# Optimization experiments

Hardware: AMD Instinct MI355X
Metric: run time of the kernel (lower is better)

## Reference

```python
import jax, jax.numpy as jnp
import numpy as np

B, S, D = 4, 2048, 1024
H = 16
DH = D // H


def setup_inputs() -> dict:
    key = jax.random.key(0)
    ks = jax.random.split(key, 9)
    s = 0.02
    return {
        "x": jax.random.normal(ks[0], (B, S, D), dtype=jnp.float32),
        "Wq": jax.random.normal(ks[1], (D, D), dtype=jnp.float32) * s,
        "bq": jax.random.normal(ks[2], (D,), dtype=jnp.float32) * s,
        "Wk": jax.random.normal(ks[3], (D, D), dtype=jnp.float32) * s,
        "bk": jax.random.normal(ks[4], (D,), dtype=jnp.float32) * s,
        "Wv": jax.random.normal(ks[5], (D, D), dtype=jnp.float32) * s,
        "bv": jax.random.normal(ks[6], (D,), dtype=jnp.float32) * s,
        "Wo": jax.random.normal(ks[7], (D, D), dtype=jnp.float32) * s,
        "bo": jax.random.normal(ks[8], (D,), dtype=jnp.float32) * s,
    }


def _split_heads(t):
    # [B,S,D] -> [B,H,S,DH]
    b, s, d = t.shape
    return t.reshape(b, s, H, DH).transpose(0, 2, 1, 3)


def reference(x, Wq, bq, Wk, bk, Wv, bv, Wo, bo):
    q = _split_heads(x @ Wq.T + bq)
    k = _split_heads(x @ Wk.T + bk)
    v = _split_heads(x @ Wv.T + bv)
    scale = 1.0 / np.sqrt(DH).astype(np.float32)
    scores = jnp.einsum("bhqd,bhkd->bhqk", q, k) * scale  # [B,H,S,S]
    s = scores.shape[-2]
    causal = jnp.tril(jnp.ones((s, s), dtype=bool))
    scores = jnp.where(causal[None, None], scores, -jnp.inf)
    probs = jax.nn.softmax(scores, axis=-1)
    out = jnp.einsum("bhqk,bhkd->bhqd", probs, v)  # [B,H,S,DH]
    out = out.transpose(0, 2, 1, 3).reshape(x.shape[0], s, D)
    return out @ Wo.T + bo
```

## Files before the change

kernel.cpp:

```cpp
#include <hip/hip_runtime.h>
#include <hip/hip_bf16.h>
#include <cstdint>
#include <cstddef>


typedef unsigned short u16;
typedef __bf16 bf16x8 __attribute__((ext_vector_type(8)));
typedef float  f32x4  __attribute__((ext_vector_type(4)));

__device__ __forceinline__ u16 f2bf(float f) {
  unsigned u = __float_as_uint(f);
  unsigned r = u + 0x7fffu + ((u >> 16) & 1u);
  return (u16)(r >> 16);
}

__device__ __forceinline__ void llds16(const u16* g, u16* l) {
  __builtin_amdgcn_global_load_lds(
      (const __attribute__((address_space(1))) void*)g,
      (__attribute__((address_space(3))) void*)l, 16, 0, 0);
}

__global__ void cast_all_kernel(const float* __restrict__ x,
                                const float* __restrict__ Wq, const float* __restrict__ Wk,
                                const float* __restrict__ Wv, const float* __restrict__ Wo,
                                u16* __restrict__ xb, u16* __restrict__ wqkv,
                                u16* __restrict__ wo) {
  const int bid = (int)blockIdx.x;
  const int tid = threadIdx.x;
  if (bid < 8192) {
    const int i = (bid << 8) + tid;
    float4 f = ((const float4*)x)[i];
    ushort4 u;
    u.x = f2bf(f.x); u.y = f2bf(f.y); u.z = f2bf(f.z); u.w = f2bf(f.w);
    ((ushort4*)xb)[i] = u;
  } else {
    const int j = ((bid - 8192) << 8) + tid;
    const int w = j >> 18;
    const int idx = j & 262143;
    const float* src = (w == 0) ? Wq : (w == 1) ? Wk : (w == 2) ? Wv : Wo;
    u16* dst = (w == 3) ? wo : (wqkv + (w << 20));
    float4 f = ((const float4*)src)[idx];
    ushort4 u;
    u.x = f2bf(f.x); u.y = f2bf(f.y); u.z = f2bf(f.z); u.w = f2bf(f.w);
    ((ushort4*)dst)[idx] = u;
  }
}

__global__ __launch_bounds__(512) void gemm_qkv_256(
    const u16* __restrict__ A, const u16* __restrict__ Bw,
    const float* __restrict__ b0, const float* __restrict__ b1, const float* __restrict__ b2,
    u16* __restrict__ qkv_out, u16* __restrict__ vT_out)
{
  __shared__ u16 lds[57344];

  const int tid = threadIdx.x;
  const int lane = tid & 63;
  const int wave = tid >> 6;

  const int bid = (int)blockIdx.x;
  const int xcd = bid & 7;
  const int idx = bid >> 3;
  const int mt = (xcd << 2) | (idx & 3);
  const int nt = idx >> 2;
  const int m0 = mt << 8;
  const int n0 = nt * 192;

  const int warp_m = wave >> 2;
  const int warp_n = wave & 3;
  const int wm = warp_m << 7;
  const int wn = warp_n * 48;
  const int fr = lane & 15;
  const int g  = lane >> 4;

  const int srow = tid >> 3;
  const int schk = ((tid & 7) ^ (srow & 7)) << 3;
  const u16* pA = A  + (size_t)(m0 + srow) * 1024 + schk;
  const u16* pB = Bw + (size_t)(n0 + srow) * 1024 + schk;

  const int rsw0 = ((g    ) ^ (fr & 7)) << 3;
  const int rsw1 = ((g ^ 4) ^ (fr & 7)) << 3;

  const u16* Ab0 = lds + (size_t)(wm + fr) * 64;
  const u16* Bb0 = lds + 16384 + (size_t)(wn + fr) * 64;
  const u16* Ab1 = Ab0 + 28672;
  const u16* Bb1 = Bb0 + 28672;

  f32x4 acc[8][3];
  const f32x4 zero = {0.f, 0.f, 0.f, 0.f};
#pragma unroll
  for (int i = 0; i < 8; i++)
#pragma unroll
    for (int j = 0; j < 3; j++) acc[i][j] = zero;

  bf16x8 a_[4][2];
  bf16x8 b_[3][2];

  auto stageA = [&](int kt, int buf, int half) {
    const u16* src = pA + (size_t)half * 131072 + (kt << 6);
    u16* dst = lds + buf * 28672 + half * 8192 + tid * 8;
    llds16(src, dst);
    llds16(src + 65536, dst + 4096);
  };
  auto stageB0 = [&](int kt, int buf) {
    const u16* src = pB + (kt << 6);
    u16* dst = lds + buf * 28672 + 16384 + tid * 8;
    llds16(src, dst);
    llds16(src + 65536, dst + 4096);
  };
  auto stageB1 = [&](int kt, int buf) {
    const u16* src = pB + 131072 + (kt << 6);
    u16* dst = lds + buf * 28672 + 24576 + tid * 8;
    llds16(src, dst);
  };
  auto loadA4 = [&](const u16* Ab, int ib) {
#pragma unroll
    for (int ii = 0; ii < 4; ii++) {
      const u16* r = Ab + (ib + ii) * 1024;
      a_[ii][0] = *(const bf16x8*)(r + rsw0);
      a_[ii][1] = *(const bf16x8*)(r + rsw1);
    }
  };
  auto loadB = [&](const u16* Bb, int j0, int nj) {
#pragma unroll
    for (int jj = 0; jj < 3; jj++) {
      if (jj < nj) {
        const u16* r = Bb + (j0 + jj) * 1024;
        b_[j0 + jj][0] = *(const bf16x8*)(r + rsw0);
        b_[j0 + jj][1] = *(const bf16x8*)(r + rsw1);
      }
    }
  };
  auto mfmaQ = [&](int ib, int j0, int nj) {
    __builtin_amdgcn_s_setprio(1);
#pragma unroll
    for (int jj = 0; jj < 3; jj++) {
      if (jj < nj) {
#pragma unroll
        for (int ii = 0; ii < 4; ii++) {
          acc[ib+ii][j0+jj] = __builtin_amdgcn_mfma_f32_16x16x32_bf16(
              a_[ii][0], b_[j0+jj][0], acc[ib+ii][j0+jj], 0, 0, 0);
          acc[ib+ii][j0+jj] = __builtin_amdgcn_mfma_f32_16x16x32_bf16(
              a_[ii][1], b_[j0+jj][1], acc[ib+ii][j0+jj], 0, 0, 0);
        }
      }
    }
    __builtin_amdgcn_s_setprio(0);
  };

  stageA(0, 0, 0);
  stageA(0, 0, 1);
  stageB0(0, 0);
  stageB1(0, 0);
  stageA(1, 1, 0);
  asm volatile("s_waitcnt vmcnt(2)" ::: "memory");
  __builtin_amdgcn_s_barrier();

  const int NTI = 8;
  for (int t = 0; t < NTI; ++t) {
    const bool st = (t < NTI - 1);
    const int ka = 2 * t + 1;
    const int kb = 2 * t + 2;
    const int kc = 2 * t + 3;

    loadA4(Ab0, 0); loadB(Bb0, 0, 2);
    stageA(ka, 1, 1);
    __builtin_amdgcn_s_barrier();
    mfmaQ(0, 0, 2);
    __builtin_amdgcn_s_barrier();
    loadB(Bb0, 2, 1);
    stageB0(ka, 1);
    __builtin_amdgcn_s_barrier();
    mfmaQ(0, 2, 1);
    __builtin_amdgcn_s_barrier();
    loadA4(Ab0, 4);
    stageB1(ka, 1);
    __builtin_amdgcn_s_barrier();
    mfmaQ(4, 2, 1);
    __builtin_amdgcn_s_barrier();
    if (st) stageA(kb, 0, 0);
    __builtin_amdgcn_s_barrier();
    mfmaQ(4, 0, 2);
    if (st) { asm volatile("s_waitcnt vmcnt(2)" ::: "memory"); }
    else    { asm volatile("s_waitcnt vmcnt(0)" ::: "memory"); }
    __builtin_amdgcn_s_barrier();

    loadA4(Ab1, 0); loadB(Bb1, 0, 2);
    if (st) stageA(kb, 0, 1);
    __builtin_amdgcn_s_barrier();
    mfmaQ(0, 0, 2);
    __builtin_amdgcn_s_barrier();
    loadB(Bb1, 2, 1);
    if (st) stageB0(kb, 0);
    __builtin_amdgcn_s_barrier();
    mfmaQ(0, 2, 1);
    __builtin_amdgcn_s_barrier();
    loadA4(Ab1, 4);
    if (st) stageB1(kb, 0);
    __builtin_amdgcn_s_barrier();
    mfmaQ(4, 2, 1);
    __builtin_amdgcn_s_barrier();
    if (st) stageA(kc, 1, 0);
    __builtin_amdgcn_s_barrier();
    mfmaQ(4, 0, 2);
    if (st) { asm volatile("s_waitcnt vmcnt(2)" ::: "memory"); }
    __builtin_amdgcn_s_barrier();
  }

  __syncthreads();
  const int bI  = m0 >> 11;
  const int s0m = m0 & 2047;
  const int vs0 = (n0 >= 2048) ? 0 : ((n0 + 192 <= 2048) ? 192 : (2048 - n0));

  if (vs0 > 0) {
#pragma unroll
    for (int j = 0; j < 3; j++) {
      const int cl = wn + j * 16 + fr;
      if (cl < vs0) {
        const int ncol = n0 + cl;
        const int which = ncol >> 10;
        const float bb = ((which == 0) ? b0 : b1)[ncol & 1023];
        const float post = (which == 0) ? 0.18033688011f : 1.0f;
#pragma unroll
        for (int i = 0; i < 8; i++) {
#pragma unroll
          for (int r = 0; r < 4; r++) {
            const int row = wm + i * 16 + g * 4 + r;
            lds[row * 200 + cl] = f2bf((acc[i][j][r] + bb) * post);
          }
        }
      }
    }
    __syncthreads();
    const int part = tid & 7;
#pragma unroll
    for (int p = 0; p < 12; p++) {
      const int hc = p >> 2;
      if (hc * 64 < vs0) {
        const int ml = ((p & 3) << 6) + (tid >> 3);
        const int ncol0 = n0 + hc * 64;
        const int which = ncol0 >> 10;
        const int h = (ncol0 >> 6) & 15;
        const bf16x8 v = *(const bf16x8*)(lds + ml * 200 + hc * 64 + part * 8);
        *(bf16x8*)(qkv_out + (size_t)which * 8388608 +
                   ((size_t)(bI * 16 + h) * 2048 + s0m + ml) * 64 + part * 8) = v;
      }
    }
  }

  if (vs0 < 192) {
    __syncthreads();
#pragma unroll
    for (int j = 0; j < 3; j++) {
      const int cl = wn + j * 16 + fr;
      const int clv = cl - vs0;
      if (clv >= 0) {
        const int ncol = n0 + cl;
        const float bb = b2[ncol & 1023];
#pragma unroll
        for (int i = 0; i < 8; i++) {
#pragma unroll
          for (int r = 0; r < 4; r++) {
            const int row = wm + i * 16 + g * 4 + r;
            lds[clv * 264 + row] = f2bf(acc[i][j][r] + bb);
          }
        }
      }
    }
    __syncthreads();
    const int vcols = 192 - vs0;
    const int mg = tid & 31;
    const int cidx = tid >> 5;
    for (int cc = cidx; cc < vcols; cc += 16) {
      const int ncol = n0 + vs0 + cc;
      const int h = (ncol >> 6) & 15;
      const int dh = ncol & 63;
      const bf16x8 v = *(const bf16x8*)(lds + cc * 264 + mg * 8);
      *(bf16x8*)(vT_out + ((size_t)(bI * 16 + h) * 64 + dh) * 2048 + s0m + mg * 8) = v;
    }
  }
}

__global__ __launch_bounds__(512) void gemm_o_256(
    const u16* __restrict__ A, const u16* __restrict__ Bw,
    const float* __restrict__ bo, float* __restrict__ out)
{
  __shared__ u16 lds[49152];

  const int tid = threadIdx.x;
  const int lane = tid & 63;
  const int wave = tid >> 6;

  const int bid = (int)blockIdx.x;
  const int xcd = bid & 7;
  const int idx = bid >> 3;
  const int mt = (xcd << 2) | (idx & 3);
  const int nt = idx >> 2;
  const int m0 = mt << 8;
  const int n0 = nt << 7;

  const int warp_m = wave >> 2;
  const int warp_n = wave & 3;
  const int wm = warp_m << 7;
  const int wn = warp_n << 5;
  const int fr = lane & 15;
  const int g  = lane >> 4;

  const int srow = tid >> 3;
  const int schk = ((tid & 7) ^ (srow & 7)) << 3;
  const u16* pA = A  + (size_t)(m0 + srow) * 1024 + schk;
  const u16* pB = Bw + (size_t)(n0 + srow) * 1024 + schk;

  const int rsw0 = ((g    ) ^ (fr & 7)) << 3;
  const int rsw1 = ((g ^ 4) ^ (fr & 7)) << 3;

  const u16* Ab0 = lds + (size_t)(wm + fr) * 64;
  const u16* Bb0 = lds + 16384 + (size_t)(wn + fr) * 64;
  const u16* Ab1 = Ab0 + 24576;
  const u16* Bb1 = Bb0 + 24576;

  f32x4 acc[8][2];
  const f32x4 zero = {0.f, 0.f, 0.f, 0.f};
#pragma unroll
  for (int i = 0; i < 8; i++)
#pragma unroll
    for (int j = 0; j < 2; j++) acc[i][j] = zero;

  bf16x8 a_[8][2];
  bf16x8 b_[2][2];

  auto stageA = [&](int kt, int buf, int half) {
    const u16* src = pA + (size_t)half * 131072 + (kt << 6);
    u16* dst = lds + buf * 24576 + half * 8192 + tid * 8;
    llds16(src, dst);
    llds16(src + 65536, dst + 4096);
  };
  auto stageB = [&](int kt, int buf) {
    const u16* src = pB + (kt << 6);
    u16* dst = lds + buf * 24576 + 16384 + tid * 8;
    llds16(src, dst);
    llds16(src + 65536, dst + 4096);
  };
  auto loadA4 = [&](const u16* Ab, int ib) {
#pragma unroll
    for (int ii = 0; ii < 4; ii++) {
      const u16* r = Ab + (ib + ii) * 1024;
      a_[ib + ii][0] = *(const bf16x8*)(r + rsw0);
      a_[ib + ii][1] = *(const bf16x8*)(r + rsw1);
    }
  };
  auto loadB2 = [&](const u16* Bb) {
#pragma unroll
    for (int jj = 0; jj < 2; jj++) {
      const u16* r = Bb + jj * 1024;
      b_[jj][0] = *(const bf16x8*)(r + rsw0);
      b_[jj][1] = *(const bf16x8*)(r + rsw1);
    }
  };
  auto mfma16 = [&](int ib) {
    __builtin_amdgcn_s_setprio(1);
#pragma unroll
    for (int jj = 0; jj < 2; jj++)
#pragma unroll
      for (int ii = 0; ii < 4; ii++) {
        acc[ib+ii][jj] = __builtin_amdgcn_mfma_f32_16x16x32_bf16(
            a_[ib+ii][0], b_[jj][0], acc[ib+ii][jj], 0, 0, 0);
        acc[ib+ii][jj] = __builtin_amdgcn_mfma_f32_16x16x32_bf16(
            a_[ib+ii][1], b_[jj][1], acc[ib+ii][jj], 0, 0, 0);
      }
    __builtin_amdgcn_s_setprio(0);
  };
  auto mfma8 = [&](int ib, int jj) {
    __builtin_amdgcn_s_setprio(1);
#pragma unroll
    for (int ii = 0; ii < 4; ii++) {
      acc[ib+ii][jj] = __builtin_amdgcn_mfma_f32_16x16x32_bf16(
          a_[ib+ii][0], b_[jj][0], acc[ib+ii][jj], 0, 0, 0);
      acc[ib+ii][jj] = __builtin_amdgcn_mfma_f32_16x16x32_bf16(
          a_[ib+ii][1], b_[jj][1], acc[ib+ii][jj], 0, 0, 0);
    }
    __builtin_amdgcn_s_setprio(0);
  };

  stageA(0, 0, 0);
  stageA(0, 0, 1);
  stageB(0, 0);
  stageA(1, 1, 0);
  asm volatile("s_waitcnt vmcnt(2)" ::: "memory");
  __builtin_amdgcn_s_barrier();

  const int NTI = 8;
  for (int t = 0; t < NTI; ++t) {
    const bool st = (t < NTI - 1);
    const int ka = 2 * t + 1;
    const int kb = 2 * t + 2;
    const int kc = 2 * t + 3;

    loadA4(Ab0, 0); loadB2(Bb0);
    stageA(ka, 1, 1);
    __builtin_amdgcn_s_barrier();
    mfma16(0);
    __builtin_amdgcn_s_barrier();
    loadA4(Ab0, 4);
    stageB(ka, 1);
    __builtin_amdgcn_s_barrier();
    mfma8(4, 0);
    __builtin_amdgcn_s_barrier();
    if (st) stageA(kb, 0, 0);
    __builtin_amdgcn_s_barrier();
    mfma8(4, 1);
    if (st) { asm volatile("s_waitcnt vmcnt(2)" ::: "memory"); }
    else    { asm volatile("s_waitcnt vmcnt(0)" ::: "memory"); }
    __builtin_amdgcn_s_barrier();

    loadA4(Ab1, 0); loadB2(Bb1);
    if (st) stageA(kb, 0, 1);
    __builtin_amdgcn_s_barrier();
    mfma16(0);
    __builtin_amdgcn_s_barrier();
    loadA4(Ab1, 4);
    if (st) stageB(kb, 0);
    __builtin_amdgcn_s_barrier();
    mfma8(4, 0);
    __builtin_amdgcn_s_barrier();
    if (st) stageA(kc, 1, 0);
    __builtin_amdgcn_s_barrier();
    mfma8(4, 1);
    if (st) { asm volatile("s_waitcnt vmcnt(2)" ::: "memory"); }
    __builtin_amdgcn_s_barrier();
  }

#pragma unroll
  for (int j = 0; j < 2; j++) {
    const int n = n0 + wn + j * 16 + fr;
    const float bb = bo[n];
#pragma unroll
    for (int i = 0; i < 8; i++) {
#pragma unroll
      for (int r = 0; r < 4; r++) {
        const int m = m0 + wm + i * 16 + g * 4 + r;
        out[(size_t)m * 1024 + n] = acc[i][j][r] + bb;
      }
    }
  }
}

__global__ __launch_bounds__(256, 3) void attn_fa(
    const u16* __restrict__ Qb, const u16* __restrict__ Kb,
    const u16* __restrict__ VT, u16* __restrict__ Ob)
{
  __shared__ u16 k_s[2 * 4096];
  __shared__ u16 v_s[2 * 4096];
  __shared__ u16 p_s[128 * 72];
  __shared__ float l_s[128];

  const int tid = threadIdx.x;
  const int lane = tid & 63;
  const int wave = tid >> 6;
  const int bid = (int)blockIdx.x;
  const int qt = 15 - (bid >> 6);
  const int bh = (((bid >> 3) & 7) << 3) | (bid & 7);
  const size_t head = (size_t)bh << 17;
  const int fr = lane & 15;
  const int g = lane >> 4;
  const int k8 = g << 3;
  const int q0 = qt << 7;
  const int wrow = wave << 5;

  if (qt >= 14)     __builtin_amdgcn_s_setprio(2);
  else if (qt >= 8) __builtin_amdgcn_s_setprio(1);

  bf16x8 aq[2][2];
#pragma unroll
  for (int f = 0; f < 2; f++) {
    const u16* qp = Qb + head + (size_t)(q0 + wrow + (f << 4) + fr) * 64;
    aq[f][0] = *(const bf16x8*)(qp + k8);
    aq[f][1] = *(const bf16x8*)(qp + 32 + k8);
  }

  const int r0 = tid >> 3, c0 = tid & 7;
  const int r1 = 32 + r0;
  const int koff0 = r0 * 64 + (((c0 ^ r0) & 7) << 3);
  const int koff1 = r1 * 64 + (((c0 ^ r1) & 7) << 3);
  const int voff0 = r0 * 2048 + (((c0 ^ r0) & 7) << 3);
  const int voff1 = r1 * 2048 + (((c0 ^ r1) & 7) << 3);
  int kaddr[4][2], vaddr[2][4];
#pragma unroll
  for (int j = 0; j < 4; j++) {
    const int kn = (j << 4) + fr;
    kaddr[j][0] = kn * 64 + (((g ^ kn) & 7) << 3);
    kaddr[j][1] = kn * 64 + ((((g + 4) ^ kn) & 7) << 3);
#pragma unroll
    for (int s2 = 0; s2 < 2; s2++)
      vaddr[s2][j] = kn * 64 + ((((s2 << 2) + g) ^ (kn & 7)) << 3);
  }
  u16* const prow0 = p_s + (wrow + fr) * 72;
  u16* const prow1 = p_s + (wrow + 16 + fr) * 72;
  const u16* Kbase = Kb + head;
  const u16* Vbase = VT + head;

  auto issueK = [&](int jt2, int buf) {
    const u16* Kt = Kbase + ((size_t)jt2 << 12);
    llds16(Kt + koff0, k_s + (buf << 12) + tid * 8);
    llds16(Kt + koff1, k_s + (buf << 12) + 2048 + tid * 8);
  };
  auto issueV = [&](int jt2, int buf) {
    const u16* Vt = Vbase + (jt2 << 6);
    llds16(Vt + voff0, v_s + (buf << 12) + tid * 8);
    llds16(Vt + voff1, v_s + (buf << 12) + 2048 + tid * 8);
  };

  f32x4 o_acc[2][4];
  const f32x4 zero = {0.f, 0.f, 0.f, 0.f};
#pragma unroll
  for (int f = 0; f < 2; f++)
#pragma unroll
    for (int j = 0; j < 4; j++) o_acc[f][j] = zero;
  float l_run[2] = {0.f, 0.f};

  const int jmax = 2 * qt + 1;
  const int jt_diag = 2 * qt + (wave >> 1);

  auto do_pv = [&](const u16* vs) {
#pragma unroll
    for (int s2 = 0; s2 < 2; s2++) {
      const bf16x8 ap0 = *(const bf16x8*)(prow0 + (s2 << 5) + k8);
      const bf16x8 ap1 = *(const bf16x8*)(prow1 + (s2 << 5) + k8);
#pragma unroll
      for (int j = 0; j < 4; j++) {
        const bf16x8 bv = *(const bf16x8*)(vs + vaddr[s2][j]);
        o_acc[0][j] = __builtin_amdgcn_mfma_f32_16x16x32_bf16(ap0, bv, o_acc[0][j], 0, 0, 0);
        o_acc[1][j] = __builtin_amdgcn_mfma_f32_16x16x32_bf16(ap1, bv, o_acc[1][j], 0, 0, 0);
      }
    }
  };

  auto do_s = [&](const u16* ks, bool dodiag, int jt) {
    f32x4 s_acc[2][4];
#pragma unroll
    for (int f = 0; f < 2; f++)
#pragma unroll
      for (int j = 0; j < 4; j++) s_acc[f][j] = zero;
#pragma unroll
    for (int j = 0; j < 4; j++) {
      const bf16x8 ka0 = *(const bf16x8*)(ks + kaddr[j][0]);
      const bf16x8 ka1 = *(const bf16x8*)(ks + kaddr[j][1]);
      s_acc[0][j] = __builtin_amdgcn_mfma_f32_16x16x32_bf16(ka0, aq[0][0], s_acc[0][j], 0, 0, 0);
      s_acc[0][j] = __builtin_amdgcn_mfma_f32_16x16x32_bf16(ka1, aq[0][1], s_acc[0][j], 0, 0, 0);
      s_acc[1][j] = __builtin_amdgcn_mfma_f32_16x16x32_bf16(ka0, aq[1][0], s_acc[1][j], 0, 0, 0);
      s_acc[1][j] = __builtin_amdgcn_mfma_f32_16x16x32_bf16(ka1, aq[1][1], s_acc[1][j], 0, 0, 0);
    }
#pragma unroll
    for (int f = 0; f < 2; f++) {
      const int qa = q0 + wrow + (f << 4) + fr;
      u16* prow = (f == 0) ? prow0 : prow1;
      if (dodiag) {
#pragma unroll
        for (int j = 0; j < 4; j++) {
          const int kb = (jt << 6) + (j << 4) + (g << 2);
          float p0 = (kb + 0 > qa) ? 0.f : __builtin_amdgcn_exp2f(s_acc[f][j][0]);
          float p1 = (kb + 1 > qa) ? 0.f : __builtin_amdgcn_exp2f(s_acc[f][j][1]);
          float p2 = (kb + 2 > qa) ? 0.f : __builtin_amdgcn_exp2f(s_acc[f][j][2]);
          float p3 = (kb + 3 > qa) ? 0.f : __builtin_amdgcn_exp2f(s_acc[f][j][3]);
          l_run[f] += (p0 + p1) + (p2 + p3);
          union { __hip_bfloat162 h; unsigned u; } ca, cb;
          ca.h = __float22bfloat162_rn(make_float2(p0, p1));
          cb.h = __float22bfloat162_rn(make_float2(p2, p3));
          *(uint2*)(prow + (j << 4) + (g << 2)) = make_uint2(ca.u, cb.u);
        }
      } else {
#pragma unroll
        for (int j = 0; j < 4; j++) {
          float p0 = __builtin_amdgcn_exp2f(s_acc[f][j][0]);
          float p1 = __builtin_amdgcn_exp2f(s_acc[f][j][1]);
          float p2 = __builtin_amdgcn_exp2f(s_acc[f][j][2]);
          float p3 = __builtin_amdgcn_exp2f(s_acc[f][j][3]);
          l_run[f] += (p0 + p1) + (p2 + p3);
          union { __hip_bfloat162 h; unsigned u; } ca, cb;
          ca.h = __float22bfloat162_rn(make_float2(p0, p1));
          cb.h = __float22bfloat162_rn(make_float2(p2, p3));
          *(uint2*)(prow + (j << 4) + (g << 2)) = make_uint2(ca.u, cb.u);
        }
      }
    }
  };

  issueK(0, 0);

  for (int jt = 0; jt <= jmax; jt++) {
    const int kb = jt & 1;
    __syncthreads();
    if (jt < jmax) issueK(jt + 1, kb ^ 1);
    issueV(jt, kb);
    if (jt > 0 && jt - 1 <= jt_diag) do_pv(v_s + ((kb ^ 1) << 12));
    if (jt <= jt_diag) do_s(k_s + (kb << 12), jt == jt_diag, jt);
  }
  __syncthreads();
  if (jt_diag == jmax) do_pv(v_s + ((jmax & 1) << 12));

#pragma unroll
  for (int f = 0; f < 2; f++) {
    float l = l_run[f];
    l += __shfl_xor(l, 16);
    l += __shfl_xor(l, 32);
    if (g == 0) l_s[wrow + (f << 4) + fr] = l;
  }
  const int b = bh >> 4, h = bh & 15;
#pragma unroll
  for (int f = 0; f < 2; f++) {
#pragma unroll
    for (int r = 0; r < 4; r++) {
      const int qloc = wrow + (f << 4) + (g << 2) + r;
      const float inv = 1.f / l_s[qloc];
      const int q_abs = q0 + qloc;
#pragma unroll
      for (int j = 0; j < 4; j++)
        Ob[((size_t)b * 2048 + q_abs) * 1024 + (h << 6) + (j << 4) + fr] =
            f2bf(o_acc[f][j][r] * inv);
    }
  }
}

extern "C" void kernel_launch(void* const* d_in, const int* in_sizes, int n_in,
                              void* d_out, int out_size, void* d_ws, size_t ws_size,
                              hipStream_t stream) {
  const float* x  = (const float*)d_in[0];
  const float* Wq = (const float*)d_in[1];
  const float* bq = (const float*)d_in[2];
  const float* Wk = (const float*)d_in[3];
  const float* bk = (const float*)d_in[4];
  const float* Wv = (const float*)d_in[5];
  const float* bv = (const float*)d_in[6];
  const float* Wo = (const float*)d_in[7];
  const float* bo = (const float*)d_in[8];
  float* out = (float*)d_out;

  char* ws = (char*)d_ws;
  u16* xb    = (u16*)(ws);
  u16* attnb = (u16*)(ws);
  u16* wqkv  = (u16*)(ws + 16777216);
  u16* wo    = (u16*)(ws + 23068672);
  u16* qkv   = (u16*)(ws + 25165824);
  u16* vT    = (u16*)(ws + 58720256);

  cast_all_kernel<<<12288, 256, 0, stream>>>(x, Wq, Wk, Wv, Wo, xb, wqkv, wo);

  gemm_qkv_256<<<dim3(512), 512, 0, stream>>>(xb, wqkv, bq, bk, bv, qkv, vT);

  attn_fa<<<dim3(1024), 256, 0, stream>>>(qkv, qkv + 8388608, vT, attnb);

  gemm_o_256<<<dim3(256), 512, 0, stream>>>(attnb, wo, bo, out);
}
```

Before: 231.8 us.

## Triple-buffer K/V tiles in flash attention with deeper prefetch and vmcnt waits

Switches the attention kernel's K and V LDS staging from double to triple buffering. K is prefetched two tiles ahead and V one tile ahead, and the per-iteration __syncthreads is replaced by a partial vmcnt wait plus a barrier. Launch bounds drop from 3 to 2 blocks per CU to fit the larger LDS footprint. The aim is to hide global-to-LDS load latency better, at the cost of occupancy and extra redundant loads at the tail (the prefetch index is clamped to jmax).

```diff
diff --git a/kernel.cpp b/kernel.cpp
--- a/kernel.cpp
+++ b/kernel.cpp
@@ -444,12 +444,12 @@
   }
 }
 
-__global__ __launch_bounds__(256, 3) void attn_fa(
+__global__ __launch_bounds__(256, 2) void attn_fa(
     const u16* __restrict__ Qb, const u16* __restrict__ Kb,
     const u16* __restrict__ VT, u16* __restrict__ Ob)
 {
-  __shared__ u16 k_s[2 * 4096];
-  __shared__ u16 v_s[2 * 4096];
+  __shared__ u16 k_s[3 * 4096];
+  __shared__ u16 v_s[3 * 4096];
   __shared__ u16 p_s[128 * 72];
   __shared__ float l_s[128];
 
@@ -498,15 +498,15 @@
   const u16* Kbase = Kb + head;
   const u16* Vbase = VT + head;
 
-  auto issueK = [&](int jt2, int buf) {
+  auto issueK = [&](int jt2, int slot) {
     const u16* Kt = Kbase + ((size_t)jt2 << 12);
-    llds16(Kt + koff0, k_s + (buf << 12) + tid * 8);
-    llds16(Kt + koff1, k_s + (buf << 12) + 2048 + tid * 8);
-  };
-  auto issueV = [&](int jt2, int buf) {
+    llds16(Kt + koff0, k_s + slot * 4096 + tid * 8);
+    llds16(Kt + koff1, k_s + slot * 4096 + 2048 + tid * 8);
+  };
+  auto issueV = [&](int jt2, int slot) {
     const u16* Vt = Vbase + (jt2 << 6);
-    llds16(Vt + voff0, v_s + (buf << 12) + tid * 8);
-    llds16(Vt + voff1, v_s + (buf << 12) + 2048 + tid * 8);
+    llds16(Vt + voff0, v_s + slot * 4096 + tid * 8);
+    llds16(Vt + voff1, v_s + slot * 4096 + 2048 + tid * 8);
   };
 
   f32x4 o_acc[2][4];
@@ -585,17 +585,25 @@
   };
 
   issueK(0, 0);
-
+  issueK(1, 1);
+  issueV(0, 0);
+  asm volatile("s_waitcnt vmcnt(4)" ::: "memory");
+  __builtin_amdgcn_s_barrier();
+
+  int kw = 2, vw = 1, kr = 0, vr = 2;
   for (int jt = 0; jt <= jmax; jt++) {
-    const int kb = jt & 1;
-    __syncthreads();
-    if (jt < jmax) issueK(jt + 1, kb ^ 1);
-    issueV(jt, kb);
-    if (jt > 0 && jt - 1 <= jt_diag) do_pv(v_s + ((kb ^ 1) << 12));
-    if (jt <= jt_diag) do_s(k_s + (kb << 12), jt == jt_diag, jt);
-  }
-  __syncthreads();
-  if (jt_diag == jmax) do_pv(v_s + ((jmax & 1) << 12));
+    issueK((jt + 2 <= jmax) ? jt + 2 : jmax, kw);
+    issueV((jt + 1 <= jmax) ? jt + 1 : jmax, vw);
+    if (jt > 0 && jt - 1 <= jt_diag) do_pv(v_s + vr * 4096);
+    if (jt <= jt_diag) do_s(k_s + kr * 4096, jt == jt_diag, jt);
+    asm volatile("s_waitcnt vmcnt(4)" ::: "memory");
+    __builtin_amdgcn_s_barrier();
+    kw = (kw == 2) ? 0 : kw + 1;
+    vw = (vw == 2) ? 0 : vw + 1;
+    kr = (kr == 2) ? 0 : kr + 1;
+    vr = (vr == 2) ? 0 : vr + 1;
+  }
+  if (jt_diag == jmax) do_pv(v_s + vr * 4096);
 
 #pragma unroll
   for (int f = 0; f < 2; f++) {
```

New measurement: 246.7 us. 6.4% more time.
